# Kernel tuning notes

Hardware: AMD Instinct MI355X
Metric: run time of the kernel (lower is better)

Reference implementation:

```python
import jax, jax.numpy as jnp
import numpy as np

DIM = 4194304
EPS = 1e-24


def setup_inputs() -> dict:
    key = jax.random.key(0)
    ks = jax.random.split(key, 17)
    dim = DIM
    s = 0.3  # weight scale ~ kaiming for small fan-in
    inp = {
        "gradient": jax.random.normal(ks[0], (dim,), jnp.float32),
        "x_prev": jax.random.normal(ks[1], (dim,), jnp.float32),
        "x_curr": jax.random.normal(ks[2], (dim,), jnp.float32),
        "loss_curr": jax.random.uniform(ks[3], (1,), jnp.float32),
        "loss_prev": jax.random.uniform(ks[4], (1,), jnp.float32),
        "Wc1": s * jax.random.normal(ks[5], (10, 3), jnp.float32),
        "Wc2": s * jax.random.normal(ks[6], (10, 10), jnp.float32),
        "Wc3": s * jax.random.normal(ks[7], (10, 10), jnp.float32),
        "Wc4": s * jax.random.normal(ks[8], (10, 10), jnp.float32),
        "Wc5": s * jax.random.normal(ks[9], (10, 10), jnp.float32),
        "Wc6": s * jax.random.normal(ks[10], (10, 10), jnp.float32),
        "Wc7": s * jax.random.normal(ks[11], (1, 10), jnp.float32),
        "Wl1": s * jax.random.normal(ks[12], (8, 4), jnp.float32),
        "Wl2": s * jax.random.normal(ks[13], (8, 8), jnp.float32),
        "Wl3": s * jax.random.normal(ks[14], (8, 8), jnp.float32),
        "Wl4": s * jax.random.normal(ks[15], (8, 8), jnp.float32),
        "Wl5": s * jax.random.normal(ks[16], (1, 8), jnp.float32),
    }
    return inp


def reference(gradient, x_prev, x_curr, loss_curr, loss_prev,
              Wc1, Wc2, Wc3, Wc4, Wc5, Wc6, Wc7,
              Wl1, Wl2, Wl3, Wl4, Wl5):
    relu = jax.nn.relu

    g_norm = jnp.linalg.norm(gradient)
    g = jnp.where(g_norm > EPS, gradient / g_norm, gradient)

    momentum = x_curr - x_prev
    m_norm = jnp.linalg.norm(momentum)
    m = jnp.where(m_norm > EPS, momentum / m_norm, momentum)

    # coefficients MLP on log(1 + scalar features); losses are detached in torch
    feats = jnp.log1p(jnp.stack([
        g_norm,
        m_norm,
        jax.lax.stop_gradient(loss_curr[0]),
        jax.lax.stop_gradient(loss_prev[0]),
    ]))  # [4]
    h = relu(Wl1 @ feats)
    h = relu(Wl2 @ h)
    h = relu(Wl3 @ h)
    h = Wl4 @ h
    step_size = Wl5 @ h  # [1]

    # direction network: 1x1 convs over the parameter dimension -> channel matmuls
    x = jnp.stack([g, m, g * m], axis=0)  # [3, dim]
    d = Wc1 @ x          # conv1 (no activation)
    d = Wc2 @ d          # conv2
    d = relu(d)
    d = relu(Wc3 @ d)
    d = relu(Wc4 @ d)
    d = relu(Wc5 @ d)
    d = Wc6 @ d          # conv6 (no activation)
    d = Wc7 @ d          # conv7 -> [1, dim]
    direction = d.reshape(-1)  # [dim]

    return x_curr - step_size * direction
```

## Files before the change

### kernel.cpp

```cpp
#include <hip/hip_runtime.h>
#include <math.h>
#include <stdint.h>

#define DIM 4194304
#define RBLOCKS 1024
#define RTHREADS 256
#define FBLOCKS 2048
#define FTHREADS 256
#define TOTTH (FBLOCKS * FTHREADS)
#define PASSES (DIM / TOTTH)
#define EPSF 1e-24f
#define SCALE 256.0f

#define WS_PART 0
#define WS_W21 2048
#define WS_W3 2176
#define WS_W4 2304
#define WS_W5 2432
#define WS_W67 2560

typedef uint32_t u32;
typedef __fp16 fp16x2 __attribute__((ext_vector_type(2)));
typedef __fp16 half8 __attribute__((ext_vector_type(8)));
typedef float f32x4 __attribute__((ext_vector_type(4)));
typedef uint32_t u32x2 __attribute__((ext_vector_type(2)));
typedef uint32_t u32x4 __attribute__((ext_vector_type(4)));

__device__ __forceinline__ u32 pack2u(float a, float b) {
    fp16x2 r = __builtin_amdgcn_cvt_pkrtz(a, b);
    return __builtin_bit_cast(u32, r);
}

__device__ __forceinline__ f32x4 mfma32(half8 a, half8 b, f32x4 c) {
    return __builtin_amdgcn_mfma_f32_16x16x32_f16(a, b, c, 0, 0, 0);
}
__device__ __forceinline__ half8 relucvt8(f32x4 a) {
    fp16x2 z2 = {(__fp16)0.f, (__fp16)0.f};
    fp16x2 c0 = __builtin_amdgcn_cvt_pkrtz(a[0], a[1]);
    fp16x2 c1 = __builtin_amdgcn_cvt_pkrtz(a[2], a[3]);
    c0 = __builtin_elementwise_max(c0, z2);
    c1 = __builtin_elementwise_max(c1, z2);
    u32x4 r = {__builtin_bit_cast(u32, c0), __builtin_bit_cast(u32, c1), 0u, 0u};
    return __builtin_bit_cast(half8, r);
}

__global__ __launch_bounds__(RTHREADS) void k_reduce(
    const float* __restrict__ grad, const float* __restrict__ xp, const float* __restrict__ xc,
    const float* __restrict__ Wc1, const float* __restrict__ Wc2, const float* __restrict__ Wc3,
    const float* __restrict__ Wc4, const float* __restrict__ Wc5, const float* __restrict__ Wc6,
    const float* __restrict__ Wc7, float* __restrict__ ws) {
    if (blockIdx.x == 0) {
        u32* wsu = (u32*)ws;
        int t = threadIdx.x;
        if (t < 128) {
            int lane = t >> 1, d = t & 1;
            int m = lane & 15, gg = lane >> 4;
            int k0 = 4 * gg + 2 * d;
            float a0 = 0.f, a1 = 0.f;
            if (m < 10 && k0 < 3) {
                for (int j = 0; j < 10; ++j) a0 += Wc2[m * 10 + j] * Wc1[j * 3 + k0];
                if (k0 == 2) a0 *= (1.f / SCALE);
            }
            if (m < 10 && k0 + 1 < 3) {
                for (int j = 0; j < 10; ++j) a1 += Wc2[m * 10 + j] * Wc1[j * 3 + k0 + 1];
                if (k0 + 1 == 2) a1 *= (1.f / SCALE);
            }
            wsu[WS_W21 + t] = pack2u(a0, a1);
            float v0, v1;
            v0 = (m < 10 && k0 < 10) ? Wc3[m * 10 + k0] : 0.f;
            v1 = (m < 10 && k0 + 1 < 10) ? Wc3[m * 10 + k0 + 1] : 0.f;
            wsu[WS_W3 + t] = pack2u(v0, v1);
            v0 = (m < 10 && k0 < 10) ? Wc4[m * 10 + k0] : 0.f;
            v1 = (m < 10 && k0 + 1 < 10) ? Wc4[m * 10 + k0 + 1] : 0.f;
            wsu[WS_W4 + t] = pack2u(v0, v1);
            v0 = (m < 10 && k0 < 10) ? Wc5[m * 10 + k0] : 0.f;
            v1 = (m < 10 && k0 + 1 < 10) ? Wc5[m * 10 + k0 + 1] : 0.f;
            wsu[WS_W5 + t] = pack2u(v0, v1);
        }
        if (t >= 128 && t < 144) {
            int j = t - 128;
            float w = 0.f;
            if (j < 10)
                for (int k = 0; k < 10; ++k) w += Wc7[k] * Wc6[k * 10 + j];
            ws[WS_W67 + j] = w;
        }
    }
    const float4* g4 = reinterpret_cast<const float4*>(grad);
    const float4* p4 = reinterpret_cast<const float4*>(xp);
    const float4* c4 = reinterpret_cast<const float4*>(xc);
    int tid = blockIdx.x * RTHREADS + threadIdx.x;
    float sg = 0.f, sm = 0.f;
    constexpr int STRIDE = RBLOCKS * RTHREADS;
#pragma unroll
    for (int it = 0; it < (DIM / 4) / STRIDE; ++it) {
        int i = tid + it * STRIDE;
        float4 gv = g4[i];
        float4 pv = p4[i];
        float4 cv = c4[i];
        sg += gv.x * gv.x + gv.y * gv.y + gv.z * gv.z + gv.w * gv.w;
        float mx = cv.x - pv.x, my = cv.y - pv.y, mz = cv.z - pv.z, mw = cv.w - pv.w;
        sm += mx * mx + my * my + mz * mz + mw * mw;
    }
#pragma unroll
    for (int off = 32; off > 0; off >>= 1) {
        sg += __shfl_down(sg, off);
        sm += __shfl_down(sm, off);
    }
    __shared__ float wg[4], wm[4];
    int wave = threadIdx.x >> 6;
    if ((threadIdx.x & 63) == 0) {
        wg[wave] = sg;
        wm[wave] = sm;
    }
    __syncthreads();
    if (threadIdx.x == 0) {
        ws[WS_PART + 2 * blockIdx.x]     = wg[0] + wg[1] + wg[2] + wg[3];
        ws[WS_PART + 2 * blockIdx.x + 1] = wm[0] + wm[1] + wm[2] + wm[3];
    }
}

__global__ __launch_bounds__(FTHREADS, 4) void k_fused(
    const float* __restrict__ grad, const float* __restrict__ xp, const float* __restrict__ xc,
    const float* __restrict__ loss_curr, const float* __restrict__ loss_prev,
    const float* __restrict__ Wl1, const float* __restrict__ Wl2, const float* __restrict__ Wl3,
    const float* __restrict__ Wl4, const float* __restrict__ Wl5,
    const float* __restrict__ ws, float* __restrict__ out) {
    __shared__ float sc[3];
    __shared__ float red[8];
    const int tid = threadIdx.x;

    {
        float fg = 0.f, fm = 0.f;
        for (int i = tid; i < RBLOCKS; i += FTHREADS) {
            fg += ws[WS_PART + 2 * i];
            fm += ws[WS_PART + 2 * i + 1];
        }
#pragma unroll
        for (int off = 32; off > 0; off >>= 1) {
            fg += __shfl_down(fg, off);
            fm += __shfl_down(fm, off);
        }
        int wv = tid >> 6;
        if ((tid & 63) == 0) {
            red[wv] = fg;
            red[4 + wv] = fm;
        }
        __syncthreads();
        if (tid == 0) {
            float g2 = red[0] + red[1] + red[2] + red[3];
            float m2 = red[4] + red[5] + red[6] + red[7];
            float g_norm = sqrtf(g2), m_norm = sqrtf(m2);
            float g_inv = (g_norm > EPSF) ? 1.f / g_norm : 1.f;
            float m_inv = (m_norm > EPSF) ? 1.f / m_norm : 1.f;
            float feats[4] = {log1pf(g_norm), log1pf(m_norm), log1pf(loss_curr[0]),
                              log1pf(loss_prev[0])};
            float h1[8], h2_[8], h3[8], h4[8];
#pragma unroll
            for (int o = 0; o < 8; ++o) {
                float acc = 0.f;
                for (int i = 0; i < 4; ++i) acc += Wl1[o * 4 + i] * feats[i];
                h1[o] = fmaxf(acc, 0.f);
            }
#pragma unroll
            for (int o = 0; o < 8; ++o) {
                float acc = 0.f;
                for (int i = 0; i < 8; ++i) acc += Wl2[o * 8 + i] * h1[i];
                h2_[o] = fmaxf(acc, 0.f);
            }
#pragma unroll
            for (int o = 0; o < 8; ++o) {
                float acc = 0.f;
                for (int i = 0; i < 8; ++i) acc += Wl3[o * 8 + i] * h2_[i];
                h3[o] = fmaxf(acc, 0.f);
            }
#pragma unroll
            for (int o = 0; o < 8; ++o) {
                float acc = 0.f;
                for (int i = 0; i < 8; ++i) acc += Wl4[o * 8 + i] * h3[i];
                h4[o] = acc;
            }
            float step = 0.f;
            for (int i = 0; i < 8; ++i) step += Wl5[i] * h4[i];
            sc[0] = g_inv * SCALE;
            sc[1] = m_inv * SCALE;
            sc[2] = step * (1.f / SCALE);
        }
        __syncthreads();
    }
    const float gs = sc[0], ms = sc[1], step_eff = sc[2];

    const u32* wsu = (const u32*)ws;
    const int lane = tid & 63;
    const int n = lane & 15, g = lane >> 4;
#define LOADFRAG(NAME, OFS)                                                    \
    half8 NAME;                                                                \
    {                                                                          \
        u32x2 lo = ((const u32x2*)(wsu + (OFS)))[lane];                        \
        u32x4 fr = {lo[0], lo[1], 0u, 0u};                                     \
        NAME = __builtin_bit_cast(half8, fr);                                  \
    }
    LOADFRAG(w21f, WS_W21)
    LOADFRAG(w3f, WS_W3)
    LOADFRAG(w4f, WS_W4)
    LOADFRAG(w5f, WS_W5)
#undef LOADFRAG
    half8 w67f;
    {
        const float* w67p = ws + WS_W67;
        u32x4 fr = {pack2u(w67p[4 * g], w67p[4 * g + 1]),
                    pack2u(w67p[4 * g + 2], w67p[4 * g + 3]), 0u, 0u};
        w67f = __builtin_bit_cast(half8, fr);
    }
    const f32x4 zf = {0.f, 0.f, 0.f, 0.f};

    int ebase = (blockIdx.x * (FTHREADS / 64) + (tid >> 6)) * 64 + lane;
    int e = ebase;
    float gvv = grad[e], pvv = xp[e], cvv = xc[e];
#pragma unroll
    for (int p = 0; p < PASSES; ++p) {
        int en = (p + 1 < PASSES) ? (e + TOTTH) : 0;
        float gvn = grad[en], pvn = xp[en], cvn = xc[en];

        float Gf = gvv * gs;
        float Mf = (cvv - pvv) * ms;
        float GMf = Gf * Mf;
        u32 pk0 = pack2u(Gf, Mf), pk1 = pack2u(GMf, 0.f);

        u32 b0[4], b1[4];
#pragma unroll
        for (int t = 0; t < 4; ++t) {
            int idx = (n + 16 * t) << 2;
            b0[t] = (u32)__builtin_amdgcn_ds_bpermute(idx, (int)pk0);
            b1[t] = (u32)__builtin_amdgcn_ds_bpermute(idx, (int)pk1);
        }
        f32x4 acc[4];
#pragma unroll
        for (int t = 0; t < 4; ++t) {
            u32x4 bb = {b0[t], b1[t], 0u, 0u};
            acc[t] = mfma32(w21f, __builtin_bit_cast(half8, bb), zf);
        }
#pragma unroll
        for (int t = 0; t < 4; ++t) acc[t] = mfma32(w3f, relucvt8(acc[t]), zf);
#pragma unroll
        for (int t = 0; t < 4; ++t) acc[t] = mfma32(w4f, relucvt8(acc[t]), zf);
#pragma unroll
        for (int t = 0; t < 4; ++t) acc[t] = mfma32(w5f, relucvt8(acc[t]), zf);
#pragma unroll
        for (int t = 0; t < 4; ++t) acc[t] = mfma32(w67f, relucvt8(acc[t]), zf);

        float dsel = (g == 0) ? acc[0][0] : (g == 1) ? acc[1][0] : (g == 2) ? acc[2][0]
                                                                            : acc[3][0];
        out[e] = fmaf(-step_eff, dsel, cvv);

        e = (p + 1 < PASSES) ? en : e;
        gvv = gvn;
        pvv = pvn;
        cvv = cvn;
    }
}

extern "C" void kernel_launch(void* const* d_in, const int* in_sizes, int n_in,
                              void* d_out, int out_size, void* d_ws, size_t ws_size,
                              hipStream_t stream) {
    const float* grad      = (const float*)d_in[0];
    const float* xp        = (const float*)d_in[1];
    const float* xc        = (const float*)d_in[2];
    const float* loss_curr = (const float*)d_in[3];
    const float* loss_prev = (const float*)d_in[4];
    const float* Wc1 = (const float*)d_in[5];
    const float* Wc2 = (const float*)d_in[6];
    const float* Wc3 = (const float*)d_in[7];
    const float* Wc4 = (const float*)d_in[8];
    const float* Wc5 = (const float*)d_in[9];
    const float* Wc6 = (const float*)d_in[10];
    const float* Wc7 = (const float*)d_in[11];
    const float* Wl1 = (const float*)d_in[12];
    const float* Wl2 = (const float*)d_in[13];
    const float* Wl3 = (const float*)d_in[14];
    const float* Wl4 = (const float*)d_in[15];
    const float* Wl5 = (const float*)d_in[16];

    float* ws  = (float*)d_ws;
    float* out = (float*)d_out;

    k_reduce<<<RBLOCKS, RTHREADS, 0, stream>>>(grad, xp, xc, Wc1, Wc2, Wc3, Wc4, Wc5, Wc6,
                                               Wc7, ws);
    k_fused<<<FBLOCKS, FTHREADS, 0, stream>>>(grad, xp, xc, loss_curr, loss_prev, Wl1, Wl2,
                                              Wl3, Wl4, Wl5, ws, out);
}
```

Baseline: 39.97 us.

## Prefetch all inputs as float4 before the norm reduction and vectorize stores

Each wave now owns a contiguous chunk of 512 elements and loads all of its gradient, x_prev and x_curr data as float4 at kernel entry, before reading the partial norms and running the scalar MLP. This overlaps global loads with the reduction prologue and replaces the strided scalar loads and stores with wide vector accesses. The eight element slots are run through the MFMA chain in sequence and the results are written back as float4. Register pressure goes up because 24 floats are held live across the prologue.

After: 47.31 us. +18.4%, slower.

```diff
diff --git a/kernel.cpp b/kernel.cpp
--- a/kernel.cpp
+++ b/kernel.cpp
@@ -7,8 +7,6 @@
 #define RTHREADS 256
 #define FBLOCKS 2048
 #define FTHREADS 256
-#define TOTTH (FBLOCKS * FTHREADS)
-#define PASSES (DIM / TOTTH)
 #define EPSF 1e-24f
 #define SCALE 256.0f
 
@@ -128,6 +126,16 @@
     __shared__ float sc[3];
     __shared__ float red[8];
     const int tid = threadIdx.x;
+    const int lane = tid & 63;
+
+    const float4* g4 = reinterpret_cast<const float4*>(grad);
+    const float4* p4 = reinterpret_cast<const float4*>(xp);
+    const float4* c4 = reinterpret_cast<const float4*>(xc);
+    const int wave_gid = blockIdx.x * (FTHREADS / 64) + (tid >> 6);
+    const int wb = wave_gid * 128;
+    float4 gA = g4[wb + lane], gB = g4[wb + 64 + lane];
+    float4 pA = p4[wb + lane], pB = p4[wb + 64 + lane];
+    float4 cA = c4[wb + lane], cB = c4[wb + 64 + lane];
 
     {
         float fg = 0.f, fm = 0.f;
@@ -190,7 +198,6 @@
     const float gs = sc[0], ms = sc[1], step_eff = sc[2];
 
     const u32* wsu = (const u32*)ws;
-    const int lane = tid & 63;
     const int n = lane & 15, g = lane >> 4;
 #define LOADFRAG(NAME, OFS)                                                    \
     half8 NAME;                                                                \
@@ -213,25 +220,32 @@
     }
     const f32x4 zf = {0.f, 0.f, 0.f, 0.f};
 
-    int ebase = (blockIdx.x * (FTHREADS / 64) + (tid >> 6)) * 64 + lane;
-    int e = ebase;
-    float gvv = grad[e], pvv = xp[e], cvv = xc[e];
-#pragma unroll
-    for (int p = 0; p < PASSES; ++p) {
-        int en = (p + 1 < PASSES) ? (e + TOTTH) : 0;
-        float gvn = grad[en], pvn = xp[en], cvn = xc[en];
-
-        float Gf = gvv * gs;
-        float Mf = (cvv - pvv) * ms;
-        float GMf = Gf * Mf;
-        u32 pk0 = pack2u(Gf, Mf), pk1 = pack2u(GMf, 0.f);
-
+    u32 pk0s[8], pk1s[8];
+    {
+        float Ga[4] = {gA.x * gs, gA.y * gs, gA.z * gs, gA.w * gs};
+        float Ma[4] = {(cA.x - pA.x) * ms, (cA.y - pA.y) * ms, (cA.z - pA.z) * ms,
+                       (cA.w - pA.w) * ms};
+        float Gb[4] = {gB.x * gs, gB.y * gs, gB.z * gs, gB.w * gs};
+        float Mb[4] = {(cB.x - pB.x) * ms, (cB.y - pB.y) * ms, (cB.z - pB.z) * ms,
+                       (cB.w - pB.w) * ms};
+#pragma unroll
+        for (int s = 0; s < 4; ++s) {
+            pk0s[s] = pack2u(Ga[s], Ma[s]);
+            pk1s[s] = pack2u(Ga[s] * Ma[s], 0.f);
+            pk0s[4 + s] = pack2u(Gb[s], Mb[s]);
+            pk1s[4 + s] = pack2u(Gb[s] * Mb[s], 0.f);
+        }
+    }
+
+    float dres[8];
+#pragma unroll
+    for (int j = 0; j < 8; ++j) {
         u32 b0[4], b1[4];
 #pragma unroll
         for (int t = 0; t < 4; ++t) {
             int idx = (n + 16 * t) << 2;
-            b0[t] = (u32)__builtin_amdgcn_ds_bpermute(idx, (int)pk0);
-            b1[t] = (u32)__builtin_amdgcn_ds_bpermute(idx, (int)pk1);
+            b0[t] = (u32)__builtin_amdgcn_ds_bpermute(idx, (int)pk0s[j]);
+            b1[t] = (u32)__builtin_amdgcn_ds_bpermute(idx, (int)pk1s[j]);
         }
         f32x4 acc[4];
 #pragma unroll
@@ -247,16 +261,22 @@
         for (int t = 0; t < 4; ++t) acc[t] = mfma32(w5f, relucvt8(acc[t]), zf);
 #pragma unroll
         for (int t = 0; t < 4; ++t) acc[t] = mfma32(w67f, relucvt8(acc[t]), zf);
-
-        float dsel = (g == 0) ? acc[0][0] : (g == 1) ? acc[1][0] : (g == 2) ? acc[2][0]
-                                                                            : acc[3][0];
-        out[e] = fmaf(-step_eff, dsel, cvv);
-
-        e = (p + 1 < PASSES) ? en : e;
-        gvv = gvn;
-        pvv = pvn;
-        cvv = cvn;
-    }
+        dres[j] = (g == 0) ? acc[0][0] : (g == 1) ? acc[1][0] : (g == 2) ? acc[2][0]
+                                                                         : acc[3][0];
+    }
+
+    float4* o4 = reinterpret_cast<float4*>(out);
+    float4 ovA, ovB;
+    ovA.x = fmaf(-step_eff, dres[0], cA.x);
+    ovA.y = fmaf(-step_eff, dres[1], cA.y);
+    ovA.z = fmaf(-step_eff, dres[2], cA.z);
+    ovA.w = fmaf(-step_eff, dres[3], cA.w);
+    ovB.x = fmaf(-step_eff, dres[4], cB.x);
+    ovB.y = fmaf(-step_eff, dres[5], cB.y);
+    ovB.z = fmaf(-step_eff, dres[6], cB.z);
+    ovB.w = fmaf(-step_eff, dres[7], cB.w);
+    o4[wb + lane] = ovA;
+    o4[wb + 64 + lane] = ovB;
 }
 
 extern "C" void kernel_launch(void* const* d_in, const int* in_sizes, int n_in,
```

## Raise occupancy, parallelize scalar MLP across lanes, split MFMA chain into halves

Applied to the files above, without the earlier changes.

Raises launch bounds from 4 to 8 waves-per-SIMD target so the compiler must fit more blocks per CU. To cut register pressure, the per-pass MFMA chain now processes two tiles at a time in two stages instead of four at once. The serial single-thread coefficient MLP is replaced by an 8-lane version using shuffles, shortening the per-block prologue. The tighter register budget risks spills or less instruction-level parallelism in the MFMA chain.

Measured after the change: 38.88 us. 1.03x faster.

```diff
diff --git a/kernel.cpp b/kernel.cpp
--- a/kernel.cpp
+++ b/kernel.cpp
@@ -119,7 +119,7 @@
     }
 }
 
-__global__ __launch_bounds__(FTHREADS, 4) void k_fused(
+__global__ __launch_bounds__(FTHREADS, 8) void k_fused(
     const float* __restrict__ grad, const float* __restrict__ xp, const float* __restrict__ xc,
     const float* __restrict__ loss_curr, const float* __restrict__ loss_prev,
     const float* __restrict__ Wl1, const float* __restrict__ Wl2, const float* __restrict__ Wl3,
@@ -128,6 +128,7 @@
     __shared__ float sc[3];
     __shared__ float red[8];
     const int tid = threadIdx.x;
+    const int lane = tid & 63;
 
     {
         float fg = 0.f, fm = 0.f;
@@ -146,51 +147,44 @@
             red[4 + wv] = fm;
         }
         __syncthreads();
-        if (tid == 0) {
+        if (tid < 64) {
             float g2 = red[0] + red[1] + red[2] + red[3];
             float m2 = red[4] + red[5] + red[6] + red[7];
             float g_norm = sqrtf(g2), m_norm = sqrtf(m2);
             float g_inv = (g_norm > EPSF) ? 1.f / g_norm : 1.f;
             float m_inv = (m_norm > EPSF) ? 1.f / m_norm : 1.f;
-            float feats[4] = {log1pf(g_norm), log1pf(m_norm), log1pf(loss_curr[0]),
-                              log1pf(loss_prev[0])};
-            float h1[8], h2_[8], h3[8], h4[8];
-#pragma unroll
-            for (int o = 0; o < 8; ++o) {
-                float acc = 0.f;
-                for (int i = 0; i < 4; ++i) acc += Wl1[o * 4 + i] * feats[i];
-                h1[o] = fmaxf(acc, 0.f);
-            }
-#pragma unroll
-            for (int o = 0; o < 8; ++o) {
-                float acc = 0.f;
-                for (int i = 0; i < 8; ++i) acc += Wl2[o * 8 + i] * h1[i];
-                h2_[o] = fmaxf(acc, 0.f);
-            }
-#pragma unroll
-            for (int o = 0; o < 8; ++o) {
-                float acc = 0.f;
-                for (int i = 0; i < 8; ++i) acc += Wl3[o * 8 + i] * h2_[i];
-                h3[o] = fmaxf(acc, 0.f);
-            }
-#pragma unroll
-            for (int o = 0; o < 8; ++o) {
-                float acc = 0.f;
-                for (int i = 0; i < 8; ++i) acc += Wl4[o * 8 + i] * h3[i];
-                h4[o] = acc;
-            }
+            float f0 = log1pf(g_norm), f1 = log1pf(m_norm);
+            float f2 = log1pf(loss_curr[0]), f3 = log1pf(loss_prev[0]);
+            int o = tid & 7;
+            float h = fmaxf(Wl1[o * 4] * f0 + Wl1[o * 4 + 1] * f1 + Wl1[o * 4 + 2] * f2 +
+                                Wl1[o * 4 + 3] * f3,
+                            0.f);
+            float acc = 0.f;
+#pragma unroll
+            for (int i = 0; i < 8; ++i) acc += Wl2[o * 8 + i] * __shfl(h, i);
+            h = fmaxf(acc, 0.f);
+            acc = 0.f;
+#pragma unroll
+            for (int i = 0; i < 8; ++i) acc += Wl3[o * 8 + i] * __shfl(h, i);
+            h = fmaxf(acc, 0.f);
+            acc = 0.f;
+#pragma unroll
+            for (int i = 0; i < 8; ++i) acc += Wl4[o * 8 + i] * __shfl(h, i);
+            h = acc;
             float step = 0.f;
-            for (int i = 0; i < 8; ++i) step += Wl5[i] * h4[i];
-            sc[0] = g_inv * SCALE;
-            sc[1] = m_inv * SCALE;
-            sc[2] = step * (1.f / SCALE);
+#pragma unroll
+            for (int i = 0; i < 8; ++i) step += Wl5[i] * __shfl(h, i);
+            if (tid == 0) {
+                sc[0] = g_inv * SCALE;
+                sc[1] = m_inv * SCALE;
+                sc[2] = step * (1.f / SCALE);
+            }
         }
         __syncthreads();
     }
     const float gs = sc[0], ms = sc[1], step_eff = sc[2];
 
     const u32* wsu = (const u32*)ws;
-    const int lane = tid & 63;
     const int n = lane & 15, g = lane >> 4;
 #define LOADFRAG(NAME, OFS)                                                    \
     half8 NAME;                                                                \
@@ -226,30 +220,37 @@
         float GMf = Gf * Mf;
         u32 pk0 = pack2u(Gf, Mf), pk1 = pack2u(GMf, 0.f);
 
-        u32 b0[4], b1[4];
-#pragma unroll
-        for (int t = 0; t < 4; ++t) {
-            int idx = (n + 16 * t) << 2;
-            b0[t] = (u32)__builtin_amdgcn_ds_bpermute(idx, (int)pk0);
-            b1[t] = (u32)__builtin_amdgcn_ds_bpermute(idx, (int)pk1);
-        }
-        f32x4 acc[4];
-#pragma unroll
-        for (int t = 0; t < 4; ++t) {
-            u32x4 bb = {b0[t], b1[t], 0u, 0u};
-            acc[t] = mfma32(w21f, __builtin_bit_cast(half8, bb), zf);
-        }
-#pragma unroll
-        for (int t = 0; t < 4; ++t) acc[t] = mfma32(w3f, relucvt8(acc[t]), zf);
-#pragma unroll
-        for (int t = 0; t < 4; ++t) acc[t] = mfma32(w4f, relucvt8(acc[t]), zf);
-#pragma unroll
-        for (int t = 0; t < 4; ++t) acc[t] = mfma32(w5f, relucvt8(acc[t]), zf);
-#pragma unroll
-        for (int t = 0; t < 4; ++t) acc[t] = mfma32(w67f, relucvt8(acc[t]), zf);
-
-        float dsel = (g == 0) ? acc[0][0] : (g == 1) ? acc[1][0] : (g == 2) ? acc[2][0]
-                                                                            : acc[3][0];
+        float dhalf0, dhalf1;
+#pragma unroll
+        for (int st = 0; st < 2; ++st) {
+            u32 b0[2], b1[2];
+#pragma unroll
+            for (int t = 0; t < 2; ++t) {
+                int idx = (n + 16 * (2 * st + t)) << 2;
+                b0[t] = (u32)__builtin_amdgcn_ds_bpermute(idx, (int)pk0);
+                b1[t] = (u32)__builtin_amdgcn_ds_bpermute(idx, (int)pk1);
+            }
+            f32x4 acc[2];
+#pragma unroll
+            for (int t = 0; t < 2; ++t) {
+                u32x4 bb = {b0[t], b1[t], 0u, 0u};
+                acc[t] = mfma32(w21f, __builtin_bit_cast(half8, bb), zf);
+            }
+#pragma unroll
+            for (int t = 0; t < 2; ++t) acc[t] = mfma32(w3f, relucvt8(acc[t]), zf);
+#pragma unroll
+            for (int t = 0; t < 2; ++t) acc[t] = mfma32(w4f, relucvt8(acc[t]), zf);
+#pragma unroll
+            for (int t = 0; t < 2; ++t) acc[t] = mfma32(w5f, relucvt8(acc[t]), zf);
+#pragma unroll
+            for (int t = 0; t < 2; ++t) acc[t] = mfma32(w67f, relucvt8(acc[t]), zf);
+            float dsel = ((g & 1) == 0) ? acc[0][0] : acc[1][0];
+            if (st == 0)
+                dhalf0 = dsel;
+            else
+                dhalf1 = dsel;
+        }
+        float dsel = (g < 2) ? dhalf0 : dhalf1;
         out[e] = fmaf(-step_eff, dsel, cvv);
 
         e = (p + 1 < PASSES) ? en : e;
```

## Hoist first loads, compute G*M after permute, split MFMA chain into halves

Applied to the files above, without the earlier changes.

Issues the first-pass global loads before the norm reduction so their latency overlaps the reduction and MLP setup. The g*m product is now formed after the bpermute with a packed fp16 multiply, halving the bpermute count per pass. The four-tile MFMA chain is processed in two halves to lower live accumulator registers, trading some instruction-level parallelism for register pressure. The scalar MLP now runs across a whole wave with lane 0 writing the result, and its inner loops are fully unrolled. Forming the product in fp16 rather than fp32 changes rounding slightly.

New measurement: 41.12 us. +2.9%, slower.

```diff
diff --git a/kernel.cpp b/kernel.cpp
--- a/kernel.cpp
+++ b/kernel.cpp
@@ -28,6 +28,10 @@
 
 __device__ __forceinline__ u32 pack2u(float a, float b) {
     fp16x2 r = __builtin_amdgcn_cvt_pkrtz(a, b);
+    return __builtin_bit_cast(u32, r);
+}
+__device__ __forceinline__ u32 pkmul(u32 a, u32 b) {
+    fp16x2 r = __builtin_bit_cast(fp16x2, a) * __builtin_bit_cast(fp16x2, b);
     return __builtin_bit_cast(u32, r);
 }
 
@@ -128,6 +132,10 @@
     __shared__ float sc[3];
     __shared__ float red[8];
     const int tid = threadIdx.x;
+    const int lane = tid & 63;
+
+    const int ebase = (blockIdx.x * (FTHREADS / 64) + (tid >> 6)) * 64 + lane;
+    float gvv = grad[ebase], pvv = xp[ebase], cvv = xc[ebase];
 
     {
         float fg = 0.f, fm = 0.f;
@@ -146,7 +154,7 @@
             red[4 + wv] = fm;
         }
         __syncthreads();
-        if (tid == 0) {
+        if (tid < 64) {
             float g2 = red[0] + red[1] + red[2] + red[3];
             float m2 = red[4] + red[5] + red[6] + red[7];
             float g_norm = sqrtf(g2), m_norm = sqrtf(m2);
@@ -158,39 +166,45 @@
 #pragma unroll
             for (int o = 0; o < 8; ++o) {
                 float acc = 0.f;
+#pragma unroll
                 for (int i = 0; i < 4; ++i) acc += Wl1[o * 4 + i] * feats[i];
                 h1[o] = fmaxf(acc, 0.f);
             }
 #pragma unroll
             for (int o = 0; o < 8; ++o) {
                 float acc = 0.f;
+#pragma unroll
                 for (int i = 0; i < 8; ++i) acc += Wl2[o * 8 + i] * h1[i];
                 h2_[o] = fmaxf(acc, 0.f);
             }
 #pragma unroll
             for (int o = 0; o < 8; ++o) {
                 float acc = 0.f;
+#pragma unroll
                 for (int i = 0; i < 8; ++i) acc += Wl3[o * 8 + i] * h2_[i];
                 h3[o] = fmaxf(acc, 0.f);
             }
 #pragma unroll
             for (int o = 0; o < 8; ++o) {
                 float acc = 0.f;
+#pragma unroll
                 for (int i = 0; i < 8; ++i) acc += Wl4[o * 8 + i] * h3[i];
                 h4[o] = acc;
             }
             float step = 0.f;
+#pragma unroll
             for (int i = 0; i < 8; ++i) step += Wl5[i] * h4[i];
-            sc[0] = g_inv * SCALE;
-            sc[1] = m_inv * SCALE;
-            sc[2] = step * (1.f / SCALE);
+            if (tid == 0) {
+                sc[0] = g_inv * SCALE;
+                sc[1] = m_inv * SCALE;
+                sc[2] = step * (1.f / SCALE);
+            }
         }
         __syncthreads();
     }
     const float gs = sc[0], ms = sc[1], step_eff = sc[2];
 
     const u32* wsu = (const u32*)ws;
-    const int lane = tid & 63;
     const int n = lane & 15, g = lane >> 4;
 #define LOADFRAG(NAME, OFS)                                                    \
     half8 NAME;                                                                \
@@ -212,10 +226,9 @@
         w67f = __builtin_bit_cast(half8, fr);
     }
     const f32x4 zf = {0.f, 0.f, 0.f, 0.f};
-
-    int ebase = (blockIdx.x * (FTHREADS / 64) + (tid >> 6)) * 64 + lane;
+    const int idxv[4] = {n << 2, (n + 16) << 2, (n + 32) << 2, (n + 48) << 2};
+
     int e = ebase;
-    float gvv = grad[e], pvv = xp[e], cvv = xc[e];
 #pragma unroll
     for (int p = 0; p < PASSES; ++p) {
         int en = (p + 1 < PASSES) ? (e + TOTTH) : 0;
@@ -223,33 +236,37 @@
 
         float Gf = gvv * gs;
         float Mf = (cvv - pvv) * ms;
-        float GMf = Gf * Mf;
-        u32 pk0 = pack2u(Gf, Mf), pk1 = pack2u(GMf, 0.f);
-
-        u32 b0[4], b1[4];
-#pragma unroll
-        for (int t = 0; t < 4; ++t) {
-            int idx = (n + 16 * t) << 2;
-            b0[t] = (u32)__builtin_amdgcn_ds_bpermute(idx, (int)pk0);
-            b1[t] = (u32)__builtin_amdgcn_ds_bpermute(idx, (int)pk1);
-        }
-        f32x4 acc[4];
-#pragma unroll
-        for (int t = 0; t < 4; ++t) {
-            u32x4 bb = {b0[t], b1[t], 0u, 0u};
-            acc[t] = mfma32(w21f, __builtin_bit_cast(half8, bb), zf);
-        }
-#pragma unroll
-        for (int t = 0; t < 4; ++t) acc[t] = mfma32(w3f, relucvt8(acc[t]), zf);
-#pragma unroll
-        for (int t = 0; t < 4; ++t) acc[t] = mfma32(w4f, relucvt8(acc[t]), zf);
-#pragma unroll
-        for (int t = 0; t < 4; ++t) acc[t] = mfma32(w5f, relucvt8(acc[t]), zf);
-#pragma unroll
-        for (int t = 0; t < 4; ++t) acc[t] = mfma32(w67f, relucvt8(acc[t]), zf);
-
-        float dsel = (g == 0) ? acc[0][0] : (g == 1) ? acc[1][0] : (g == 2) ? acc[2][0]
-                                                                            : acc[3][0];
+        u32 pk0 = pack2u(Gf, Mf);
+
+        float dhalf0, dhalf1;
+#pragma unroll
+        for (int st = 0; st < 2; ++st) {
+            u32 b0[2];
+#pragma unroll
+            for (int t = 0; t < 2; ++t)
+                b0[t] = (u32)__builtin_amdgcn_ds_bpermute(idxv[2 * st + t], (int)pk0);
+            f32x4 acc[2];
+#pragma unroll
+            for (int t = 0; t < 2; ++t) {
+                u32 b1 = pkmul(b0[t], (b0[t] >> 16) | (b0[t] << 16));
+                u32x4 bb = {b0[t], b1, 0u, 0u};
+                acc[t] = mfma32(w21f, __builtin_bit_cast(half8, bb), zf);
+            }
+#pragma unroll
+            for (int t = 0; t < 2; ++t) acc[t] = mfma32(w3f, relucvt8(acc[t]), zf);
+#pragma unroll
+            for (int t = 0; t < 2; ++t) acc[t] = mfma32(w4f, relucvt8(acc[t]), zf);
+#pragma unroll
+            for (int t = 0; t < 2; ++t) acc[t] = mfma32(w5f, relucvt8(acc[t]), zf);
+#pragma unroll
+            for (int t = 0; t < 2; ++t) acc[t] = mfma32(w67f, relucvt8(acc[t]), zf);
+            float dsel = ((g & 1) == 0) ? acc[0][0] : acc[1][0];
+            if (st == 0)
+                dhalf0 = dsel;
+            else
+                dhalf1 = dsel;
+        }
+        float dsel = (g < 2) ? dhalf0 : dhalf1;
         out[e] = fmaf(-step_eff, dsel, cvv);
 
         e = (p + 1 < PASSES) ? en : e;
```
